# Optimization experiments

Measured on AMD Instinct MI355X. Metric: run time of the kernel, lower is better.

Reference implementation:

```python
import jax, jax.numpy as jnp
import numpy as np

NH, HD = 16, 64
STRIDE = 8
TOP_K_PCT = 0.1
NEG = -1e9


def setup_inputs() -> dict:
    key = jax.random.key(0)
    ks = jax.random.split(key, 6)
    B, T, D = 1, 2048, 1024
    x = jax.random.normal(ks[0], (B, T, D), dtype=jnp.float32)
    U = jax.random.uniform(ks[1], (B, T), dtype=jnp.float32)
    s = 1.0 / np.sqrt(D)
    wq = jax.random.normal(ks[2], (NH * HD, D), dtype=jnp.float32) * s
    wk = jax.random.normal(ks[3], (NH * HD, D), dtype=jnp.float32) * s
    wv = jax.random.normal(ks[4], (NH * HD, D), dtype=jnp.float32) * s
    wo = jax.random.normal(ks[5], (D, NH * HD), dtype=jnp.float32) * s
    return {"x": x, "U": U, "wq": wq, "wk": wk, "wv": wv, "wo": wo}


def _derive_mask(Q, K, U, T):
    # downsampled scores: [B, nH, T/8, T/8]
    Qd = Q[:, :, ::STRIDE, :]
    Kd = K[:, :, ::STRIDE, :]
    scores = jnp.einsum('bhid,bhjd->bhij', Qd, Kd) * (HD ** -0.5)
    # upsample back to [B, nH, T, T] via repeat_interleave
    sf = jnp.repeat(jnp.repeat(scores, STRIDE, axis=2), STRIDE, axis=3)[:, :, :T, :T]
    u_scale = (1.0 + jnp.clip(U, 0.0, 1.0))[:, None, :, None]  # [B,1,T,1]
    sf = sf * u_scale
    k = max(1, int(T * TOP_K_PCT))
    kth = jax.lax.top_k(sf, k)[0][..., k - 1:k]  # kth-largest per row, [B,nH,T,1]
    return jax.nn.sigmoid((sf - kth) * 10.0)


def reference(x, U, wq, wk, wv, wo):
    B, T, D = x.shape
    Q = (x @ wq.T).reshape(B, T, NH, HD).transpose(0, 2, 1, 3)
    K = (x @ wk.T).reshape(B, T, NH, HD).transpose(0, 2, 1, 3)
    V = (x @ wv.T).reshape(B, T, NH, HD).transpose(0, 2, 1, 3)
    mask = _derive_mask(Q, K, U, T)
    causal = jnp.tril(jnp.ones((T, T), dtype=jnp.float32))
    mask = mask * causal[None, None, :, :]
    scores = jnp.einsum('bhid,bhjd->bhij', Q, K) * (HD ** -0.5)
    scores = scores + (1.0 - mask) * NEG
    attn = jax.nn.softmax(scores, axis=-1)
    out = jnp.einsum('bhij,bhjd->bhid', attn, V)
    out = out.transpose(0, 2, 1, 3).reshape(B, T, NH * HD)
    return out @ wo.T
```

## Files before the change

kernel.cpp:

```cpp
#include <hip/hip_runtime.h>
#include <hip/hip_bf16.h>
#include <cmath>

typedef __attribute__((ext_vector_type(8))) short bf16x8;
typedef __attribute__((ext_vector_type(4))) short bf16x4;
typedef __attribute__((ext_vector_type(4))) float f32x4;

constexpr int Tq  = 2048;
constexpr int Dm  = 1024;
constexpr int NHC = 16;
constexpr int HDC = 64;
constexpr int TDC = 256;
constexpr int KSEL = 26;
constexpr int CH  = 8;

__device__ inline ushort f2bf(float x) {
  union { float f; unsigned u; } v; v.f = x;
  return (ushort)((v.u + 0x7FFF + ((v.u >> 16) & 1)) >> 16);
}
__device__ inline float bf2f(ushort b) {
  union { unsigned u; float f; } v; v.u = ((unsigned)b) << 16;
  return v.f;
}
__device__ inline void gload16(const ushort* g, ushort* l) {
  __builtin_amdgcn_global_load_lds(
      (const __attribute__((address_space(1))) unsigned int*)g,
      (__attribute__((address_space(3))) unsigned int*)l, 16, 0, 0);
}

__global__ __launch_bounds__(256) void cast_split_all(
    const float* __restrict__ x,  const float* __restrict__ wq,
    const float* __restrict__ wk, const float* __restrict__ wv,
    const float* __restrict__ wo,
    ushort* __restrict__ xh,  ushort* __restrict__ xl,
    ushort* __restrict__ wqh, ushort* __restrict__ wql,
    ushort* __restrict__ wkh, ushort* __restrict__ wkl,
    ushort* __restrict__ wvh, ushort* __restrict__ wvl,
    ushort* __restrict__ woh, ushort* __restrict__ wol) {
  int z = blockIdx.y, blk = blockIdx.x;
  const float* src; ushort *hi, *lo;
  if (z == 0)      { src = x;  hi = xh;  lo = xl; }
  else if (z == 1) { if (blk >= 1024) return; src = wq; hi = wqh; lo = wql; }
  else if (z == 2) { if (blk >= 1024) return; src = wk; hi = wkh; lo = wkl; }
  else if (z == 3) { if (blk >= 1024) return; src = wv; hi = wvh; lo = wvl; }
  else             { if (blk >= 1024) return; src = wo; hi = woh; lo = wol; }
  int base = (blk * 256 + threadIdx.x) * 4;
  float4 v = *(const float4*)&src[base];
  ushort h0 = f2bf(v.x), h1 = f2bf(v.y), h2 = f2bf(v.z), h3 = f2bf(v.w);
  *(ushort4*)&hi[base] = make_ushort4(h0, h1, h2, h3);
  *(ushort4*)&lo[base] = make_ushort4(
      f2bf(v.x - bf2f(h0)), f2bf(v.y - bf2f(h1)),
      f2bf(v.z - bf2f(h2)), f2bf(v.w - bf2f(h3)));
}

__global__ __launch_bounds__(256, 2) void fused_gemms(
    const float* __restrict__ x, const float* __restrict__ wq,
    const float* __restrict__ wk, float* __restrict__ Qd,
    float* __restrict__ Kd, float* __restrict__ xp,
    const ushort* __restrict__ xh_, const ushort* __restrict__ xl_,
    const ushort* __restrict__ wqh_, const ushort* __restrict__ wql_,
    const ushort* __restrict__ wkh_, const ushort* __restrict__ wkl_,
    const ushort* __restrict__ wvh_, const ushort* __restrict__ wvl_,
    ushort* __restrict__ Qh, ushort* __restrict__ Ql,
    ushort* __restrict__ Kh, ushort* __restrict__ Kl,
    ushort* __restrict__ Vth) {
  __shared__ __align__(16) char smem[65536];
  int bid = blockIdx.x;
  int tid = threadIdx.x;
  if (bid < 128) {
    int mat = bid >> 6;
    int rem = bid & 63;
    int n0 = (rem & 15) * 64, m0 = (rem >> 4) * 64;
    const float* B = mat ? wk : wq;
    float* C = mat ? Kd : Qd;
    float (*As)[68] = (float(*)[68])(smem);
    float (*Bs)[68] = (float(*)[68])(smem + 32 * 68 * 4);
    int tx = tid & 15, ty = tid >> 4;
    float acc[4][4] = {};
    for (int k0 = 0; k0 < 1024; k0 += 32) {
#pragma unroll
      for (int q = 0; q < 2; ++q) {
        int f = tid * 2 + q;
        int row = f >> 3, c4 = f & 7;
        float4 av = *(const float4*)&x[(size_t)((m0 + row) * 8) * 1024 + k0 + c4 * 4];
        float4 bv = *(const float4*)&B[(size_t)(n0 + row) * 1024 + k0 + c4 * 4];
        As[c4 * 4 + 0][row] = av.x; As[c4 * 4 + 1][row] = av.y;
        As[c4 * 4 + 2][row] = av.z; As[c4 * 4 + 3][row] = av.w;
        Bs[c4 * 4 + 0][row] = bv.x; Bs[c4 * 4 + 1][row] = bv.y;
        Bs[c4 * 4 + 2][row] = bv.z; Bs[c4 * 4 + 3][row] = bv.w;
      }
      __syncthreads();
#pragma unroll
      for (int k = 0; k < 32; ++k) {
        float a[4], b[4];
#pragma unroll
        for (int i = 0; i < 4; ++i) { a[i] = As[k][ty * 4 + i]; b[i] = Bs[k][tx * 4 + i]; }
#pragma unroll
        for (int i = 0; i < 4; ++i)
#pragma unroll
          for (int j = 0; j < 4; ++j) acc[i][j] += a[i] * b[j];
      }
      __syncthreads();
    }
#pragma unroll
    for (int i = 0; i < 4; ++i)
#pragma unroll
      for (int j = 0; j < 4; ++j)
        C[(size_t)(m0 + ty * 4 + i) * 1024 + n0 + tx * 4 + j] = acc[i][j];
    return;
  }
  if (bid < 192) {
    int b = bid - 128;
    float4 s = {0.f, 0.f, 0.f, 0.f};
    for (int r = 0; r < 32; ++r) {
      float4 v = *(const float4*)&x[(size_t)(b * 32 + r) * Dm + tid * 4];
      s.x += v.x; s.y += v.y; s.z += v.z; s.w += v.w;
    }
    *(float4*)&xp[b * Dm + tid * 4] = s;
    return;
  }
  int q_ = bid - 192;
  int z = q_ >> 7, rem = q_ & 127;
  int n0 = (rem & 7) * 128, m0 = (rem >> 3) * 128;
  const ushort* Bhp = (z == 0) ? wqh_ : ((z == 1) ? wkh_ : wvh_);
  const ushort* Blp = (z == 0) ? wql_ : ((z == 1) ? wkl_ : wvl_);
  ushort (*AhS)[64] = (ushort(*)[64])(smem);
  ushort (*AlS)[64] = (ushort(*)[64])(smem + 16384);
  ushort (*BhS)[64] = (ushort(*)[64])(smem + 32768);
  ushort (*BlS)[64] = (ushort(*)[64])(smem + 49152);
  int w = tid >> 6, l = tid & 63, l15 = l & 15, lg = l >> 4;
  int qr = w >> 1, qc = w & 1;
  int lrow = l >> 3, lc8 = l & 7;
  f32x4 acc[4][4] = {};
  for (int k0 = 0; k0 < Dm; k0 += 64) {
    __syncthreads();
#pragma unroll
    for (int s = 0; s < 4; ++s) {
      int row = 32 * w + s * 8 + lrow;
      int scol = (lc8 ^ (row & 7)) * 8;
      size_t ao = (size_t)(m0 + row) * Dm + k0 + scol;
      size_t bo = (size_t)(n0 + row) * Dm + k0 + scol;
      gload16(&xh_[ao], &AhS[32 * w + s * 8][0]);
      gload16(&xl_[ao], &AlS[32 * w + s * 8][0]);
      gload16(&Bhp[bo], &BhS[32 * w + s * 8][0]);
      gload16(&Blp[bo], &BlS[32 * w + s * 8][0]);
    }
    __syncthreads();
#pragma unroll
    for (int kst = 0; kst < 2; ++kst) {
      bf16x8 ah[4], al[4], bh[4], bl[4];
#pragma unroll
      for (int i = 0; i < 4; ++i) {
        int ar = qr * 64 + i * 16 + l15;
        int sa = ((kst * 4 + lg) ^ (ar & 7)) * 8;
        ah[i] = *(const bf16x8*)&AhS[ar][sa];
        al[i] = *(const bf16x8*)&AlS[ar][sa];
        int br = qc * 64 + i * 16 + l15;
        int sb = ((kst * 4 + lg) ^ (br & 7)) * 8;
        bh[i] = *(const bf16x8*)&BhS[br][sb];
        bl[i] = *(const bf16x8*)&BlS[br][sb];
      }
#pragma unroll
      for (int i = 0; i < 4; ++i)
#pragma unroll
        for (int j = 0; j < 4; ++j) {
          acc[i][j] = __builtin_amdgcn_mfma_f32_16x16x32_bf16(ah[i], bh[j], acc[i][j], 0, 0, 0);
          acc[i][j] = __builtin_amdgcn_mfma_f32_16x16x32_bf16(al[i], bh[j], acc[i][j], 0, 0, 0);
          acc[i][j] = __builtin_amdgcn_mfma_f32_16x16x32_bf16(ah[i], bl[j], acc[i][j], 0, 0, 0);
        }
    }
  }
#pragma unroll
  for (int i = 0; i < 4; ++i)
#pragma unroll
    for (int j = 0; j < 4; ++j) {
      int r0 = m0 + qr * 64 + i * 16 + lg * 4;
      int cc = n0 + qc * 64 + j * 16 + l15;
      if (z <= 1) {
        ushort* Chi = (z == 0) ? Qh : Kh;
        ushort* Clo = (z == 0) ? Ql : Kl;
        size_t o = (size_t)(cc >> 6) * Tq * HDC + (size_t)r0 * HDC + (cc & 63);
#pragma unroll
        for (int rg = 0; rg < 4; ++rg) {
          float v = acc[i][j][rg];
          ushort hh = f2bf(v);
          Chi[o + (size_t)rg * HDC] = hh;
          Clo[o + (size_t)rg * HDC] = f2bf(v - bf2f(hh));
        }
      } else {
        bf16x4 ph;
#pragma unroll
        for (int rg = 0; rg < 4; ++rg) ph[rg] = (short)f2bf(acc[i][j][rg]);
        size_t o = (size_t)(cc >> 6) * HDC * Tq + (size_t)(cc & 63) * Tq + r0;
        *(bf16x4*)&Vth[o] = ph;
      }
    }
}

__global__ __launch_bounds__(256, 2) void gemm128_out(
    const ushort* __restrict__ Ah, const ushort* __restrict__ Al,
    const ushort* __restrict__ Bh, const ushort* __restrict__ Bl,
    float* __restrict__ Cf) {
  __shared__ ushort AhS[128][64], AlS[128][64], BhS[128][64], BlS[128][64];
  int tid = threadIdx.x, w = tid >> 6, l = tid & 63, l15 = l & 15, lg = l >> 4;
  int qr = w >> 1, qc = w & 1;
  int lrow = l >> 3, lc8 = l & 7;
  int m0 = blockIdx.y * 128, n0 = blockIdx.x * 128;
  f32x4 acc[4][4] = {};
  for (int k0 = 0; k0 < Dm; k0 += 64) {
    __syncthreads();
#pragma unroll
    for (int s = 0; s < 4; ++s) {
      int row = 32 * w + s * 8 + lrow;
      int scol = (lc8 ^ (row & 7)) * 8;
      size_t ao = (size_t)(m0 + row) * Dm + k0 + scol;
      size_t bo = (size_t)(n0 + row) * Dm + k0 + scol;
      gload16(&Ah[ao], &AhS[32 * w + s * 8][0]);
      gload16(&Al[ao], &AlS[32 * w + s * 8][0]);
      gload16(&Bh[bo], &BhS[32 * w + s * 8][0]);
      gload16(&Bl[bo], &BlS[32 * w + s * 8][0]);
    }
    __syncthreads();
#pragma unroll
    for (int kst = 0; kst < 2; ++kst) {
      bf16x8 ah[4], al[4], bh[4], bl[4];
#pragma unroll
      for (int i = 0; i < 4; ++i) {
        int ar = qr * 64 + i * 16 + l15;
        int sa = ((kst * 4 + lg) ^ (ar & 7)) * 8;
        ah[i] = *(const bf16x8*)&AhS[ar][sa];
        al[i] = *(const bf16x8*)&AlS[ar][sa];
        int br = qc * 64 + i * 16 + l15;
        int sb = ((kst * 4 + lg) ^ (br & 7)) * 8;
        bh[i] = *(const bf16x8*)&BhS[br][sb];
        bl[i] = *(const bf16x8*)&BlS[br][sb];
      }
#pragma unroll
      for (int i = 0; i < 4; ++i)
#pragma unroll
        for (int j = 0; j < 4; ++j) {
          acc[i][j] = __builtin_amdgcn_mfma_f32_16x16x32_bf16(ah[i], bh[j], acc[i][j], 0, 0, 0);
          acc[i][j] = __builtin_amdgcn_mfma_f32_16x16x32_bf16(al[i], bh[j], acc[i][j], 0, 0, 0);
          acc[i][j] = __builtin_amdgcn_mfma_f32_16x16x32_bf16(ah[i], bl[j], acc[i][j], 0, 0, 0);
        }
    }
  }
#pragma unroll
  for (int i = 0; i < 4; ++i)
#pragma unroll
    for (int j = 0; j < 4; ++j) {
      int r0 = m0 + qr * 64 + i * 16 + lg * 4;
      int cc = n0 + qc * 64 + j * 16 + l15;
#pragma unroll
      for (int rg = 0; rg < 4; ++rg)
        Cf[(size_t)(r0 + rg) * Dm + cc] = acc[i][j][rg];
    }
}

__global__ __launch_bounds__(256) void sd_kernel(
    const float* __restrict__ Qd, const float* __restrict__ Kd,
    float* __restrict__ Sd) {
  __shared__ float Qs[64][68];
  __shared__ float Ks[64][68];
  int jk0 = blockIdx.x * 64, iq0 = blockIdx.y * 64, h = blockIdx.z;
  int tid = threadIdx.x, tx = tid & 15, ty = tid >> 4;
#pragma unroll
  for (int q = 0; q < 4; ++q) {
    int f = tid * 4 + q;
    int row = f >> 4, c4 = f & 15;
    float4 q4 = *(const float4*)&Qd[(size_t)(iq0 + row) * Dm + h * HDC + c4 * 4];
    float4 k4 = *(const float4*)&Kd[(size_t)(jk0 + row) * Dm + h * HDC + c4 * 4];
    Qs[c4 * 4 + 0][row] = q4.x; Qs[c4 * 4 + 1][row] = q4.y;
    Qs[c4 * 4 + 2][row] = q4.z; Qs[c4 * 4 + 3][row] = q4.w;
    Ks[c4 * 4 + 0][row] = k4.x; Ks[c4 * 4 + 1][row] = k4.y;
    Ks[c4 * 4 + 2][row] = k4.z; Ks[c4 * 4 + 3][row] = k4.w;
  }
  __syncthreads();
  float acc[4][4] = {};
#pragma unroll
  for (int k = 0; k < 64; ++k) {
    float a[4], b[4];
#pragma unroll
    for (int i = 0; i < 4; ++i) { a[i] = Qs[k][ty * 4 + i]; b[i] = Ks[k][tx * 4 + i]; }
#pragma unroll
    for (int i = 0; i < 4; ++i)
#pragma unroll
      for (int j = 0; j < 4; ++j) acc[i][j] += a[i] * b[j];
  }
#pragma unroll
  for (int i = 0; i < 4; ++i)
#pragma unroll
    for (int j = 0; j < 4; ++j)
      Sd[(size_t)(h * TDC + iq0 + ty * 4 + i) * TDC + jk0 + tx * 4 + j] =
          acc[i][j] * 0.125f;
}

__global__ __launch_bounds__(256) void fused_kth_xm(
    const float* __restrict__ Sd, float* __restrict__ kth,
    const float* __restrict__ xp, float* __restrict__ xm) {
  int blk = blockIdx.x, tid = threadIdx.x;
  if (blk < 1024) {
    int lane = tid & 63;
    int b = blk * 4 + (tid >> 6);
    const float* row = &Sd[(size_t)b * TDC];
    float v[4];
#pragma unroll
    for (int j = 0; j < 4; ++j) v[j] = row[lane + 64 * j];
    float ans = 0.f;
    for (int it = 0; it < KSEL; ++it) {
      float lm = fmaxf(fmaxf(v[0], v[1]), fmaxf(v[2], v[3]));
#pragma unroll
      for (int off = 1; off < 64; off <<= 1) lm = fmaxf(lm, __shfl_xor(lm, off));
      if (it == KSEL - 1) { ans = lm; break; }
      unsigned long long ball =
          __ballot(v[0] == lm || v[1] == lm || v[2] == lm || v[3] == lm);
      int first = __ffsll(ball) - 1;
      if (lane == first) {
        if (v[0] == lm) v[0] = -INFINITY;
        else if (v[1] == lm) v[1] = -INFINITY;
        else if (v[2] == lm) v[2] = -INFINITY;
        else v[3] = -INFINITY;
      }
    }
    if (lane == 0) kth[b] = ans;
  } else {
    float4 s = {0.f, 0.f, 0.f, 0.f};
    for (int i = 0; i < 64; ++i) {
      float4 v = *(const float4*)&xp[i * Dm + tid * 4];
      s.x += v.x; s.y += v.y; s.z += v.z; s.w += v.w;
    }
    float4 o = {s.x * (1.f / 2048.f), s.y * (1.f / 2048.f),
                s.z * (1.f / 2048.f), s.w * (1.f / 2048.f)};
    *(float4*)&xm[tid * 4] = o;
  }
}

__global__ __launch_bounds__(256) void fused_attn_vm(
    const ushort* __restrict__ Qh, const ushort* __restrict__ Ql,
    const ushort* __restrict__ Kh, const ushort* __restrict__ Kl,
    const ushort* __restrict__ Vth, const float* __restrict__ U,
    const float* __restrict__ Sd, const float* __restrict__ kth,
    const float* __restrict__ xm, const float* __restrict__ wv,
    float* __restrict__ Vm,
    ushort* __restrict__ Pacc, float* __restrict__ Pm, float* __restrict__ Pl) {
  int pidx = blockIdx.x;
  int tid = threadIdx.x;
  if (pidx >= 1280) {
    int h = pidx - 1280;
    int r = h * 64 + (tid >> 2), q = tid & 3;
    const float* wrow = wv + (size_t)r * Dm + q * 256;
    const float* a = xm + q * 256;
    float s = 0.f;
    for (int k = 0; k < 256; k += 4) {
      float4 w4 = *(const float4*)&wrow[k];
      float4 a4 = *(const float4*)&a[k];
      s += w4.x * a4.x + w4.y * a4.y + w4.z * a4.z + w4.w * a4.w;
    }
    s += __shfl_xor(s, 1); s += __shfl_xor(s, 2);
    if (q == 0) Vm[r] = s;
    return;
  }
  int xcd = pidx & 7, idx = pidx >> 3;
  int h = xcd * 2 + (idx & 1);
  int p = idx >> 1;
  int c, qt;
  if (p < 32)      { c = 0; qt = p; }
  else if (p < 56) { c = 1; qt = p - 24; }
  else if (p < 72) { c = 2; qt = p - 40; }
  else             { c = 3; qt = p - 48; }
  int w = tid >> 6, l = tid & 63, l15 = l & 15, lg = l >> 4;
  int lrow = l >> 3, lc8 = l & 7;
  int i0 = qt * 64;
  int irow = i0 + 16 * w + l15;

  __shared__ ushort KhS[64][64], KlS[64][64], VhS[64][64];
  __shared__ ushort Ps[4][16][72];

  float uu; { float t = U[irow]; uu = 1.f + fminf(fmaxf(t, 0.f), 1.f); }
  int i8 = irow >> 3;
  float kv = kth[h * TDC + i8];
  float kvu = kv * uu;
  const float* SdRow = Sd + ((size_t)h * TDC + i8) * TDC;

  size_t qoff = ((size_t)h * Tq + irow) * HDC;
  bf16x8 qh0 = *(const bf16x8*)(Qh + qoff + lg * 8);
  bf16x8 qh1 = *(const bf16x8*)(Qh + qoff + 32 + lg * 8);
  bf16x8 ql0 = *(const bf16x8*)(Ql + qoff + lg * 8);
  bf16x8 ql1 = *(const bf16x8*)(Ql + qoff + 32 + lg * 8);

  float mrow = -INFINITY, lrow_acc = 0.f;
  f32x4 acc[4] = {};

  int jt1 = min(c * CH + CH, qt + 1);
  for (int jt = c * CH; jt < jt1; ++jt) {
    int j0 = jt * 64;
    __syncthreads();
#pragma unroll
    for (int hh = 0; hh < 2; ++hh) {
      int row = 16 * w + hh * 8 + lrow;
      int scol = (lc8 ^ (row & 7)) * 8;
      size_t ko = ((size_t)h * Tq + j0 + row) * HDC + scol;
      size_t vo = ((size_t)h * HDC + row) * Tq + j0 + scol;
      gload16(&Kh[ko], &KhS[16 * w + hh * 8][0]);
      gload16(&Kl[ko], &KlS[16 * w + hh * 8][0]);
      gload16(&Vth[vo], &VhS[16 * w + hh * 8][0]);
    }

    float pen[4];
    {
      int jb0 = (j0 >> 3) + (lg >> 1);
#pragma unroll
      for (int nt = 0; nt < 4; ++nt) {
        float sdv = SdRow[jb0 + nt * 2];
        float arg = (sdv * uu - kvu) * 10.f;
        float mk;
        if (arg >= 0.f) mk = 1.f / (1.f + expf(-arg));
        else { float e = expf(arg); mk = e / (1.f + e); }
        pen[nt] = (1.f - mk) * (-1.0e9f);
      }
    }
    __syncthreads();

    f32x4 s[4] = {};
#pragma unroll
    for (int nt = 0; nt < 4; ++nt) {
      int kr = nt * 16 + l15;
      int s0 = ((0 + lg) ^ (kr & 7)) * 8;
      int s1 = ((4 + lg) ^ (kr & 7)) * 8;
      bf16x8 ah0 = *(const bf16x8*)&KhS[kr][s0];
      bf16x8 ah1 = *(const bf16x8*)&KhS[kr][s1];
      bf16x8 al0 = *(const bf16x8*)&KlS[kr][s0];
      bf16x8 al1 = *(const bf16x8*)&KlS[kr][s1];
      s[nt] = __builtin_amdgcn_mfma_f32_16x16x32_bf16(ah0, qh0, s[nt], 0, 0, 0);
      s[nt] = __builtin_amdgcn_mfma_f32_16x16x32_bf16(ah1, qh1, s[nt], 0, 0, 0);
      s[nt] = __builtin_amdgcn_mfma_f32_16x16x32_bf16(al0, qh0, s[nt], 0, 0, 0);
      s[nt] = __builtin_amdgcn_mfma_f32_16x16x32_bf16(al1, qh1, s[nt], 0, 0, 0);
      s[nt] = __builtin_amdgcn_mfma_f32_16x16x32_bf16(ah0, ql0, s[nt], 0, 0, 0);
      s[nt] = __builtin_amdgcn_mfma_f32_16x16x32_bf16(ah1, ql1, s[nt], 0, 0, 0);
    }

    bool diag = (jt == qt);
    float lgv[4][4];
    float tmax = -INFINITY;
    if (diag) {
#pragma unroll
      for (int nt = 0; nt < 4; ++nt)
#pragma unroll
        for (int rg = 0; rg < 4; ++rg) {
          int jj = j0 + nt * 16 + lg * 4 + rg;
          float lv = s[nt][rg] * 0.125f + ((jj > irow) ? -1.0e9f : pen[nt]);
          lgv[nt][rg] = lv;
          tmax = fmaxf(tmax, lv);
        }
    } else {
#pragma unroll
      for (int nt = 0; nt < 4; ++nt)
#pragma unroll
        for (int rg = 0; rg < 4; ++rg) {
          float lv = s[nt][rg] * 0.125f + pen[nt];
          lgv[nt][rg] = lv;
          tmax = fmaxf(tmax, lv);
        }
    }
    tmax = fmaxf(tmax, __shfl_xor(tmax, 16));
    tmax = fmaxf(tmax, __shfl_xor(tmax, 32));
    float mnew = fmaxf(mrow, tmax);
    float ps = 0.f;
#pragma unroll
    for (int nt = 0; nt < 4; ++nt) {
      float p0 = __expf(lgv[nt][0] - mnew);
      float p1 = __expf(lgv[nt][1] - mnew);
      float p2 = __expf(lgv[nt][2] - mnew);
      float p3 = __expf(lgv[nt][3] - mnew);
      ps += (p0 + p1) + (p2 + p3);
      uint2 pk;
      asm("v_cvt_pk_bf16_f32 %0, %1, %2" : "=v"(pk.x) : "v"(p0), "v"(p1));
      asm("v_cvt_pk_bf16_f32 %0, %1, %2" : "=v"(pk.y) : "v"(p2), "v"(p3));
      *(uint2*)&Ps[w][l15][nt * 16 + lg * 4] = pk;
    }
    ps += __shfl_xor(ps, 16);
    ps += __shfl_xor(ps, 32);
    if (!__all(tmax <= mrow)) {
      float sc = __expf(mrow - mnew);
      lrow_acc = lrow_acc * sc + ps;
      mrow = mnew;
      float scr[4];
#pragma unroll
      for (int rg = 0; rg < 4; ++rg) scr[rg] = __shfl(sc, lg * 4 + rg);
#pragma unroll
      for (int ntd = 0; ntd < 4; ++ntd)
#pragma unroll
        for (int rg = 0; rg < 4; ++rg) acc[ntd][rg] *= scr[rg];
    } else {
      lrow_acc += ps;
    }

#pragma unroll
    for (int kst = 0; kst < 2; ++kst) {
      bf16x8 pa = *(const bf16x8*)&Ps[w][l15][kst * 32 + lg * 8];
#pragma unroll
      for (int ntd = 0; ntd < 4; ++ntd) {
        int vr = ntd * 16 + l15;
        int sv = ((kst * 4 + lg) ^ (vr & 7)) * 8;
        bf16x8 vbh = *(const bf16x8*)&VhS[vr][sv];
        acc[ntd] = __builtin_amdgcn_mfma_f32_16x16x32_bf16(pa, vbh, acc[ntd], 0, 0, 0);
      }
    }
  }

  size_t rowbase = ((size_t)c * NHC + h) * Tq + i0 + 16 * w;
  if (lg == 0) {
    Pm[rowbase + l15] = mrow;
    Pl[rowbase + l15] = lrow_acc;
  }
#pragma unroll
  for (int ntd = 0; ntd < 4; ++ntd)
#pragma unroll
    for (int rg = 0; rg < 4; ++rg)
      Pacc[(rowbase + lg * 4 + rg) * HDC + ntd * 16 + l15] = f2bf(acc[ntd][rg]);
}

__global__ __launch_bounds__(256) void attn_merge(
    const ushort* __restrict__ Pacc, const float* __restrict__ Pm,
    const float* __restrict__ Pl, const float* __restrict__ Vm,
    ushort* __restrict__ AOh, ushort* __restrict__ AOl) {
  int qt = blockIdx.x, h = blockIdx.y;
  int tid = threadIdx.x;
  int r = tid >> 2, q4 = tid & 3;
  int gi = qt * 64 + r;
  int nc = (qt >> 3) + 1;
  float M = -INFINITY, mv[4];
#pragma unroll
  for (int cc = 0; cc < 4; ++cc) {
    mv[cc] = (cc < nc) ? Pm[((size_t)cc * NHC + h) * Tq + gi] : -INFINITY;
    M = fmaxf(M, mv[cc]);
  }
  if (M == -1.0e9f) {
#pragma unroll
    for (int dd = 0; dd < 16; dd += 4) {
      int d = q4 * 16 + dd;
      float4 v = *(const float4*)&Vm[h * HDC + d];
      float vv[4] = {v.x, v.y, v.z, v.w};
      ushort4 uh, ul;
      ushort* uhp = &uh.x; ushort* ulp = &ul.x;
#pragma unroll
      for (int j = 0; j < 4; ++j) {
        ushort hh = f2bf(vv[j]);
        uhp[j] = hh; ulp[j] = f2bf(vv[j] - bf2f(hh));
      }
      *(ushort4*)&AOh[(size_t)gi * Dm + h * HDC + d] = uh;
      *(ushort4*)&AOl[(size_t)gi * Dm + h * HDC + d] = ul;
    }
    return;
  }
  float W[4], L = 0.f;
#pragma unroll
  for (int cc = 0; cc < 4; ++cc) {
    W[cc] = (cc < nc) ? __expf(mv[cc] - M) : 0.f;
    if (cc < nc) L += Pl[((size_t)cc * NHC + h) * Tq + gi] * W[cc];
  }
  float invL = 1.f / L;
#pragma unroll
  for (int dd = 0; dd < 16; dd += 4) {
    int d = q4 * 16 + dd;
    float o[4] = {0.f, 0.f, 0.f, 0.f};
    for (int cc = 0; cc < nc; ++cc) {
      bf16x4 a = *(const bf16x4*)&Pacc[(((size_t)cc * NHC + h) * Tq + gi) * HDC + d];
#pragma unroll
      for (int j = 0; j < 4; ++j) o[j] += bf2f((ushort)a[j]) * W[cc];
    }
    ushort4 uh, ul;
    ushort* uhp = &uh.x; ushort* ulp = &ul.x;
#pragma unroll
    for (int j = 0; j < 4; ++j) {
      float vv = o[j] * invL;
      ushort hh = f2bf(vv);
      uhp[j] = hh; ulp[j] = f2bf(vv - bf2f(hh));
    }
    *(ushort4*)&AOh[(size_t)gi * Dm + h * HDC + d] = uh;
    *(ushort4*)&AOl[(size_t)gi * Dm + h * HDC + d] = ul;
  }
}

extern "C" void kernel_launch(void* const* d_in, const int* in_sizes, int n_in,
                              void* d_out, int out_size, void* d_ws, size_t ws_size,
                              hipStream_t stream) {
  const float* x  = (const float*)d_in[0];
  const float* U  = (const float*)d_in[1];
  const float* wq = (const float*)d_in[2];
  const float* wk = (const float*)d_in[3];
  const float* wv = (const float*)d_in[4];
  const float* wo = (const float*)d_in[5];
  float* out = (float*)d_out;

  float* fw = (float*)d_ws;
  const size_t TD_ = (size_t)Tq * Dm;
  const size_t WW_ = (size_t)Dm * Dm;
  const size_t QD_ = (size_t)TDC * Dm;
  float* Qd  = fw;                 fw += QD_;
  float* Kd  = fw;                 fw += QD_;
  float* Sd  = fw;                 fw += (size_t)NHC * TDC * TDC;
  float* kth = fw;                 fw += 4096;
  float* Vm  = fw;                 fw += 4096;
  float* xm  = fw;                 fw += 4096;
  float* xp  = fw;                 fw += 64 * Dm;
  float* Pm  = fw;                 fw += 4 * NHC * Tq;
  float* Pl  = fw;                 fw += 4 * NHC * Tq;
  ushort* uw = (ushort*)fw;
  ushort* xh   = uw;               uw += TD_;
  ushort* xl   = uw;               uw += TD_;
  ushort* wqh  = uw;               uw += WW_;
  ushort* wql  = uw;               uw += WW_;
  ushort* wkh  = uw;               uw += WW_;
  ushort* wkl  = uw;               uw += WW_;
  ushort* wvh  = uw;               uw += WW_;
  ushort* wvl  = uw;               uw += WW_;
  ushort* woh  = uw;               uw += WW_;
  ushort* wol  = uw;               uw += WW_;
  ushort* Qh   = uw;               uw += TD_;
  ushort* Ql   = uw;               uw += TD_;
  ushort* Kh   = uw;               uw += TD_;
  ushort* Kl   = uw;               uw += TD_;
  ushort* Vth  = uw;               uw += TD_;
  ushort* Pacc = uw;               uw += (size_t)4 * NHC * Tq * HDC;
  ushort* AOh = xh;
  ushort* AOl = xl;

  dim3 bb(256);
  cast_split_all<<<dim3(2048, 5), bb, 0, stream>>>(
      x, wq, wk, wv, wo, xh, xl, wqh, wql, wkh, wkl, wvh, wvl, woh, wol);
  fused_gemms<<<dim3(576), bb, 0, stream>>>(
      x, wq, wk, Qd, Kd, xp,
      xh, xl, wqh, wql, wkh, wkl, wvh, wvl, Qh, Ql, Kh, Kl, Vth);
  sd_kernel<<<dim3(4, 4, NHC), bb, 0, stream>>>(Qd, Kd, Sd);
  fused_kth_xm<<<dim3(1025), bb, 0, stream>>>(Sd, kth, xp, xm);
  fused_attn_vm<<<dim3(1296), bb, 0, stream>>>(
      Qh, Ql, Kh, Kl, Vth, U, Sd, kth, xm, wv, Vm, Pacc, Pm, Pl);
  attn_merge<<<dim3(Tq / 64, NHC), bb, 0, stream>>>(Pacc, Pm, Pl, Vm, AOh, AOl);
  gemm128_out<<<dim3(8, 16), bb, 0, stream>>>(AOh, AOl, woh, wol, out);
}
```

Baseline: 182.4 us.

## Double-buffer downsampled QK GEMM tiles and compact cast grid

The fp32 GEMM path for the downsampled Q/K projections now uses two LDS buffers with a K-step of 16. The next tile's global loads are issued before computing on the current tile, so there is one barrier per step instead of two. The cast kernel switches from a 2D grid of 2048x5 blocks, many of which exited immediately, to a 1D grid of exactly 6144 useful blocks. Exposed memory latency should shrink and empty blocks are no longer launched, at the cost of twice as many loop iterations and extra registers held across the compute phase.

After: 181.9 us. About the same (-0.3%).

```diff
diff --git a/kernel.cpp b/kernel.cpp
--- a/kernel.cpp
+++ b/kernel.cpp
@@ -37,13 +37,17 @@
     ushort* __restrict__ wkh, ushort* __restrict__ wkl,
     ushort* __restrict__ wvh, ushort* __restrict__ wvl,
     ushort* __restrict__ woh, ushort* __restrict__ wol) {
-  int z = blockIdx.y, blk = blockIdx.x;
-  const float* src; ushort *hi, *lo;
-  if (z == 0)      { src = x;  hi = xh;  lo = xl; }
-  else if (z == 1) { if (blk >= 1024) return; src = wq; hi = wqh; lo = wql; }
-  else if (z == 2) { if (blk >= 1024) return; src = wk; hi = wkh; lo = wkl; }
-  else if (z == 3) { if (blk >= 1024) return; src = wv; hi = wvh; lo = wvl; }
-  else             { if (blk >= 1024) return; src = wo; hi = woh; lo = wol; }
+  int bid = blockIdx.x;
+  const float* src; ushort *hi, *lo; int blk;
+  if (bid < 2048)      { src = x;  hi = xh;  lo = xl;  blk = bid; }
+  else {
+    int z = (bid - 2048) >> 10;
+    blk = (bid - 2048) & 1023;
+    if (z == 0)      { src = wq; hi = wqh; lo = wql; }
+    else if (z == 1) { src = wk; hi = wkh; lo = wkl; }
+    else if (z == 2) { src = wv; hi = wvh; lo = wvl; }
+    else             { src = wo; hi = woh; lo = wol; }
+  }
   int base = (blk * 256 + threadIdx.x) * 4;
   float4 v = *(const float4*)&src[base];
   ushort h0 = f2bf(v.x), h1 = f2bf(v.y), h2 = f2bf(v.z), h3 = f2bf(v.w);
@@ -73,32 +77,50 @@
     int n0 = (rem & 15) * 64, m0 = (rem >> 4) * 64;
     const float* B = mat ? wk : wq;
     float* C = mat ? Kd : Qd;
-    float (*As)[68] = (float(*)[68])(smem);
-    float (*Bs)[68] = (float(*)[68])(smem + 32 * 68 * 4);
+    typedef float lds16x68[16][68];
+    lds16x68* As = (lds16x68*)(smem);
+    lds16x68* Bs = (lds16x68*)(smem + 2 * 16 * 68 * 4);
     int tx = tid & 15, ty = tid >> 4;
+    int srow = tid >> 2, sc4 = tid & 3;
+    const float* Arow = &x[(size_t)((m0 + srow) * 8) * 1024 + sc4 * 4];
+    const float* Brow = &B[(size_t)(n0 + srow) * 1024 + sc4 * 4];
     float acc[4][4] = {};
-    for (int k0 = 0; k0 < 1024; k0 += 32) {
-#pragma unroll
-      for (int q = 0; q < 2; ++q) {
-        int f = tid * 2 + q;
-        int row = f >> 3, c4 = f & 7;
-        float4 av = *(const float4*)&x[(size_t)((m0 + row) * 8) * 1024 + k0 + c4 * 4];
-        float4 bv = *(const float4*)&B[(size_t)(n0 + row) * 1024 + k0 + c4 * 4];
-        As[c4 * 4 + 0][row] = av.x; As[c4 * 4 + 1][row] = av.y;
-        As[c4 * 4 + 2][row] = av.z; As[c4 * 4 + 3][row] = av.w;
-        Bs[c4 * 4 + 0][row] = bv.x; Bs[c4 * 4 + 1][row] = bv.y;
-        Bs[c4 * 4 + 2][row] = bv.z; Bs[c4 * 4 + 3][row] = bv.w;
-      }
-      __syncthreads();
-#pragma unroll
-      for (int k = 0; k < 32; ++k) {
+    {
+      float4 av = *(const float4*)&Arow[0];
+      float4 bv = *(const float4*)&Brow[0];
+      As[0][sc4 * 4 + 0][srow] = av.x; As[0][sc4 * 4 + 1][srow] = av.y;
+      As[0][sc4 * 4 + 2][srow] = av.z; As[0][sc4 * 4 + 3][srow] = av.w;
+      Bs[0][sc4 * 4 + 0][srow] = bv.x; Bs[0][sc4 * 4 + 1][srow] = bv.y;
+      Bs[0][sc4 * 4 + 2][srow] = bv.z; Bs[0][sc4 * 4 + 3][srow] = bv.w;
+    }
+    __syncthreads();
+    for (int iter = 0; iter < 64; ++iter) {
+      int cbuf = iter & 1, nbuf = cbuf ^ 1;
+      bool hn = (iter + 1 < 64);
+      float4 av, bv;
+      if (hn) {
+        int k0 = (iter + 1) * 16;
+        av = *(const float4*)&Arow[k0];
+        bv = *(const float4*)&Brow[k0];
+      }
+#pragma unroll
+      for (int k = 0; k < 16; ++k) {
         float a[4], b[4];
 #pragma unroll
-        for (int i = 0; i < 4; ++i) { a[i] = As[k][ty * 4 + i]; b[i] = Bs[k][tx * 4 + i]; }
+        for (int i = 0; i < 4; ++i) {
+          a[i] = As[cbuf][k][ty * 4 + i];
+          b[i] = Bs[cbuf][k][tx * 4 + i];
+        }
 #pragma unroll
         for (int i = 0; i < 4; ++i)
 #pragma unroll
           for (int j = 0; j < 4; ++j) acc[i][j] += a[i] * b[j];
+      }
+      if (hn) {
+        As[nbuf][sc4 * 4 + 0][srow] = av.x; As[nbuf][sc4 * 4 + 1][srow] = av.y;
+        As[nbuf][sc4 * 4 + 2][srow] = av.z; As[nbuf][sc4 * 4 + 3][srow] = av.w;
+        Bs[nbuf][sc4 * 4 + 0][srow] = bv.x; Bs[nbuf][sc4 * 4 + 1][srow] = bv.y;
+        Bs[nbuf][sc4 * 4 + 2][srow] = bv.z; Bs[nbuf][sc4 * 4 + 3][srow] = bv.w;
       }
       __syncthreads();
     }
@@ -627,7 +649,7 @@
   ushort* AOl = xl;
 
   dim3 bb(256);
-  cast_split_all<<<dim3(2048, 5), bb, 0, stream>>>(
+  cast_split_all<<<dim3(6144), bb, 0, stream>>>(
       x, wq, wk, wv, wo, xh, xl, wqh, wql, wkh, wkl, wvh, wvl, woh, wol);
   fused_gemms<<<dim3(576), bb, 0, stream>>>(
       x, wq, wk, Qd, Kd, xp,
```
